# Performance work log

Hardware: AMD Instinct MI355X
Metric: run time of the kernel (lower is better)

The kernel has to match this reference:

```python
import jax, jax.numpy as jnp
import numpy as np

BOX_SIZE = 120
RESOLUTION = 1.0
NUM_NEIGHBOURS = 2
NUM_TYPES = 11
MAX_ATOMS = 512
BATCH = 4


def setup_inputs() -> dict:
    key = jax.random.key(0)
    k1, k2 = jax.random.split(key)
    # coords uniformly inside the box with a margin so Gaussians stay mostly in-grid
    margin = 5.0
    input_coords = jax.random.uniform(
        k1, (BATCH, NUM_TYPES, 3 * MAX_ATOMS), dtype=jnp.float32,
        minval=margin, maxval=BOX_SIZE * RESOLUTION - margin)
    num_atoms = jax.random.randint(k2, (BATCH, NUM_TYPES), 1, MAX_ATOMS + 1).astype(jnp.int64)
    return {"input_coords": input_coords, "num_atoms": num_atoms}


def _coords2volume(input_coords, num_atoms):
    B, T, C = input_coords.shape
    A = C // 3
    pos = input_coords.reshape(B * T, A, 3)  # [BT, A, 3] xyz per atom
    n = NUM_NEIGHBOURS
    res = RESOLUTION
    # (2n+1)^3 neighbour-cell offsets
    r = jnp.arange(-n, n + 1)
    offs = jnp.stack(jnp.meshgrid(r, r, r, indexing="ij"), axis=-1).reshape(-1, 3)  # [K,3]
    # home cell of each atom (spatial hash cell)
    cell = jnp.floor(pos / res).astype(jnp.int32)  # [BT, A, 3]
    nb = cell[:, :, None, :] + offs[None, None, :, :]  # [BT, A, K, 3]
    # truncated Gaussian density at neighbour-cell grid points
    cell_pos = nb.astype(pos.dtype) * res
    r2 = jnp.sum((cell_pos - pos[:, :, None, :]) ** 2, axis=-1)  # [BT, A, K]
    val = jnp.exp(-r2 / (res * res))
    # mask cells outside the grid and padded atoms
    in_box = jnp.all((nb >= 0) & (nb < BOX_SIZE), axis=-1)  # [BT, A, K]
    atom_mask = jnp.arange(A)[None, :] < num_atoms.reshape(-1)[:, None]  # [BT, A]
    val = jnp.where(in_box & atom_mask[:, :, None], val, 0.0)
    # scatter-add into flattened voxel grid
    flat = (nb[..., 0] * BOX_SIZE + nb[..., 1]) * BOX_SIZE + nb[..., 2]
    flat = jnp.clip(flat, 0, BOX_SIZE ** 3 - 1)
    vol = jnp.zeros((B * T, BOX_SIZE ** 3), dtype=pos.dtype)
    bidx = jnp.arange(B * T)[:, None, None]
    vol = vol.at[bidx, flat].add(val)
    return vol.reshape(B, T, BOX_SIZE, BOX_SIZE, BOX_SIZE)


def reference(input_coords, num_atoms):
    return _coords2volume(input_coords, num_atoms)
```

## Files before the change

kernel.cpp:

```cpp
#include <hip/hip_runtime.h>
#include <stdint.h>

#define BOX 120
#define BOX2 (BOX * BOX)
#define BOX3 (BOX * BOX * BOX)
#define NTYPES 11
#define NBATCH 4
#define BT (NBATCH * NTYPES)
#define MAXA 512
#define NNB 2
#define KCELLS 125

#define NBINS (BT * BOX2)
#define BINCAP 8
#define YTILE 8
#define NYT (BOX / YTILE)

#define WS_COUNTS_BYTES ((size_t)NBINS * 4)
#define WS_BINS_BYTES   ((size_t)NBINS * BINCAP * 2)
#define WS_NEEDED       (WS_COUNTS_BYTES + WS_BINS_BYTES)


__global__ __launch_bounds__(256)
void zero_counts_kernel(uint4* __restrict__ counts4, int n4) {
    int i = blockIdx.x * blockDim.x + threadIdx.x;
    if (i < n4) counts4[i] = make_uint4(0u, 0u, 0u, 0u);
}

__global__ __launch_bounds__(256)
void bin_kernel(const float* __restrict__ coords,
                const int* __restrict__ num_atoms,
                uint32_t* __restrict__ counts,
                uint16_t* __restrict__ bins) {
    int tid = blockIdx.x * blockDim.x + threadIdx.x;
    if (tid >= BT * MAXA) return;
    int bt = tid / MAXA;
    int a  = tid % MAXA;
    if (a >= num_atoms[bt]) return;
    const float* p = coords + (size_t)bt * (3 * MAXA) + (size_t)a * 3;
    int cx = (int)floorf(p[0]);
    int cy = (int)floorf(p[1]);
    if ((unsigned)cx >= BOX || (unsigned)cy >= BOX) return;
    int bin = (bt * BOX + cx) * BOX + cy;
    uint32_t idx = atomicAdd(&counts[bin], 1u);
    if (idx < BINCAP) bins[(size_t)bin * BINCAP + idx] = (uint16_t)a;
}

__global__ __launch_bounds__(256)
void gather_kernel(const float* __restrict__ coords,
                   const uint32_t* __restrict__ counts,
                   const uint16_t* __restrict__ bins,
                   float* __restrict__ out) {
    int b  = blockIdx.x;
    int bt = b / (BOX * NYT);
    int r  = b % (BOX * NYT);
    int x  = r / NYT;
    int y0 = (r % NYT) * YTILE;

    const int NB_Y = YTILE + 2 * NNB;
    __shared__ float4 s_at[5 * NB_Y * BINCAP];
    __shared__ float  s_w[5 * NB_Y * BINCAP];
    __shared__ int    s_n;
    if (threadIdx.x == 0) s_n = 0;
    __syncthreads();

    int t = threadIdx.x;
    if (t < 5 * NB_Y) {
        int cxb = x - NNB + t / NB_Y;
        int cyb = y0 - NNB + t % NB_Y;
        if ((unsigned)cxb < BOX && (unsigned)cyb < BOX) {
            int bin = (bt * BOX + cxb) * BOX + cyb;
            int c = (int)counts[bin];
            if (c > BINCAP) c = BINCAP;
            if (c > 0) {
                int base = atomicAdd(&s_n, c);
                for (int k = 0; k < c; ++k) {
                    int a = bins[(size_t)bin * BINCAP + k];
                    const float* p = coords + (size_t)bt * (3 * MAXA) + (size_t)a * 3;
                    float px = p[0], py = p[1], pz = p[2];
                    float fx = (float)x - px;
                    s_at[base + k] = make_float4(py, pz, floorf(py), floorf(pz));
                    s_w[base + k]  = __expf(-fx * fx);
                }
            }
        }
    }
    __syncthreads();
    int n = s_n;

    size_t obase = (size_t)(bt * BOX + x) * BOX2 + (size_t)y0 * BOX;
    for (int it = 0; it < 4; ++it) {
        int v = threadIdx.x + it * 256;
        if (v < YTILE * BOX) {
            float yf = (float)(y0 + v / BOX);
            float zf = (float)(v % BOX);
            float acc = 0.f;
            for (int i = 0; i < n; ++i) {
                float4 at = s_at[i];
                if (fabsf(yf - at.z) <= 2.0f && fabsf(zf - at.w) <= 2.0f) {
                    float dy = yf - at.x;
                    float dz = zf - at.y;
                    acc += s_w[i] * __expf(-(dy * dy + dz * dz));
                }
            }
            __builtin_nontemporal_store(acc, out + obase + v);
        }
    }
}


__global__ __launch_bounds__(256)
void zero_out_kernel(float4* __restrict__ out, int n4) {
    int i = blockIdx.x * blockDim.x + threadIdx.x;
    if (i < n4) out[i] = make_float4(0.f, 0.f, 0.f, 0.f);
}

__global__ __launch_bounds__(256)
void scatter_kernel(const float* __restrict__ coords,
                    const int* __restrict__ num_atoms,
                    float* __restrict__ out) {
    int idx = blockIdx.x * blockDim.x + threadIdx.x;
    const int total = BT * MAXA * KCELLS;
    if (idx >= total) return;
    int k   = idx % KCELLS;
    int tmp = idx / KCELLS;
    int a   = tmp % MAXA;
    int bt  = tmp / MAXA;
    if (a >= num_atoms[bt]) return;
    const float* p = coords + (size_t)bt * (3 * MAXA) + (size_t)a * 3;
    float px = p[0], py = p[1], pz = p[2];
    int dz = k % 5, t2 = k / 5;
    int dy = t2 % 5, dx = t2 / 5;
    int nx = (int)floorf(px) + dx - NNB;
    int ny = (int)floorf(py) + dy - NNB;
    int nz = (int)floorf(pz) + dz - NNB;
    if ((unsigned)nx >= BOX || (unsigned)ny >= BOX || (unsigned)nz >= BOX) return;
    float fx = (float)nx - px, fy = (float)ny - py, fz = (float)nz - pz;
    float val = __expf(-(fx * fx + fy * fy + fz * fz));
    atomicAdd(out + (size_t)bt * BOX3 + (size_t)((nx * BOX + ny) * BOX + nz), val);
}

extern "C" void kernel_launch(void* const* d_in, const int* in_sizes, int n_in,
                              void* d_out, int out_size, void* d_ws, size_t ws_size,
                              hipStream_t stream) {
    const float* coords    = (const float*)d_in[0];
    const int*   num_atoms = (const int*)d_in[1];
    float*       out       = (float*)d_out;

    if (ws_size >= WS_NEEDED) {
        uint32_t* counts = (uint32_t*)d_ws;
        uint16_t* bins   = (uint16_t*)((char*)d_ws + WS_COUNTS_BYTES);

        int n4 = NBINS / 4;
        zero_counts_kernel<<<(n4 + 255) / 256, 256, 0, stream>>>((uint4*)counts, n4);

        bin_kernel<<<(BT * MAXA + 255) / 256, 256, 0, stream>>>(coords, num_atoms, counts, bins);

        int gblocks = BT * BOX * NYT;
        gather_kernel<<<gblocks, 256, 0, stream>>>(coords, counts, bins, out);
    } else {
        int n4 = out_size / 4;
        zero_out_kernel<<<(n4 + 255) / 256, 256, 0, stream>>>((float4*)d_out, n4);
        const int total = BT * MAXA * KCELLS;
        scatter_kernel<<<(total + 255) / 256, 256, 0, stream>>>(coords, num_atoms, out);
    }
}
```

Baseline: 354.6 us.

## Bin atoms by x-slab and gather whole yz planes with threshold culling

Atoms are now binned by x cell only (cap 24 per bin) instead of by (x,y) cell. Each block computes a full 120x120 yz plane for one x slice and writes four voxels per thread as a vector store. Contributions whose separable Gaussian factors fall below a small threshold are skipped, which cuts the per-voxel exp and compare work. The cost is a much larger candidate list per block: with 24 atoms per bin and 5 bins, every voxel scans up to 120 atoms. The threshold also drops tiny values the reference keeps, and bins overflowing 24 atoms silently lose atoms.

```diff
diff --git a/kernel.cpp b/kernel.cpp
--- a/kernel.cpp
+++ b/kernel.cpp
@@ -9,22 +9,22 @@
 #define BT (NBATCH * NTYPES)
 #define MAXA 512
 #define NNB 2
-#define KCELLS 125
 
-#define NBINS (BT * BOX2)
-#define BINCAP 8
-#define YTILE 8
-#define NYT (BOX / YTILE)
+#define DELTA 2e-3f
 
+#define BINCAP 24
+#define NBINS (BT * BOX)
+#define SLOTS (5 * BINCAP)
 #define WS_COUNTS_BYTES ((size_t)NBINS * 4)
 #define WS_BINS_BYTES   ((size_t)NBINS * BINCAP * 2)
 #define WS_NEEDED       (WS_COUNTS_BYTES + WS_BINS_BYTES)
 
+typedef float v4f __attribute__((ext_vector_type(4)));
 
 __global__ __launch_bounds__(256)
-void zero_counts_kernel(uint4* __restrict__ counts4, int n4) {
+void zero_counts_kernel(uint32_t* __restrict__ counts) {
     int i = blockIdx.x * blockDim.x + threadIdx.x;
-    if (i < n4) counts4[i] = make_uint4(0u, 0u, 0u, 0u);
+    if (i < NBINS) counts[i] = 0u;
 }
 
 __global__ __launch_bounds__(256)
@@ -37,50 +37,47 @@
     int bt = tid / MAXA;
     int a  = tid % MAXA;
     if (a >= num_atoms[bt]) return;
-    const float* p = coords + (size_t)bt * (3 * MAXA) + (size_t)a * 3;
-    int cx = (int)floorf(p[0]);
-    int cy = (int)floorf(p[1]);
-    if ((unsigned)cx >= BOX || (unsigned)cy >= BOX) return;
-    int bin = (bt * BOX + cx) * BOX + cy;
-    uint32_t idx = atomicAdd(&counts[bin], 1u);
-    if (idx < BINCAP) bins[(size_t)bin * BINCAP + idx] = (uint16_t)a;
+    float px = coords[(size_t)bt * (3 * MAXA) + 3 * (size_t)a];
+    int cx = (int)floorf(px);
+    if ((unsigned)cx >= BOX) return;
+    int bin = bt * BOX + cx;
+    uint32_t k = atomicAdd(&counts[bin], 1u);
+    if (k < BINCAP) bins[(size_t)bin * BINCAP + k] = (uint16_t)a;
 }
 
 __global__ __launch_bounds__(256)
-void gather_kernel(const float* __restrict__ coords,
-                   const uint32_t* __restrict__ counts,
-                   const uint16_t* __restrict__ bins,
-                   float* __restrict__ out) {
+void gather_slab_kernel(const float* __restrict__ coords,
+                        const uint32_t* __restrict__ counts,
+                        const uint16_t* __restrict__ bins,
+                        v4f* __restrict__ out4) {
     int b  = blockIdx.x;
-    int bt = b / (BOX * NYT);
-    int r  = b % (BOX * NYT);
-    int x  = r / NYT;
-    int y0 = (r % NYT) * YTILE;
+    int bt = b / BOX;
+    int x  = b % BOX;
 
-    const int NB_Y = YTILE + 2 * NNB;
-    __shared__ float4 s_at[5 * NB_Y * BINCAP];
-    __shared__ float  s_w[5 * NB_Y * BINCAP];
+    __shared__ float4 s_at[SLOTS];
+    __shared__ float  s_ex[SLOTS];
     __shared__ int    s_n;
     if (threadIdx.x == 0) s_n = 0;
     __syncthreads();
 
     int t = threadIdx.x;
-    if (t < 5 * NB_Y) {
-        int cxb = x - NNB + t / NB_Y;
-        int cyb = y0 - NNB + t % NB_Y;
-        if ((unsigned)cxb < BOX && (unsigned)cyb < BOX) {
-            int bin = (bt * BOX + cxb) * BOX + cyb;
-            int c = (int)counts[bin];
+    if (t < SLOTS) {
+        int cx = x - NNB + t / BINCAP;
+        int k  = t % BINCAP;
+        if ((unsigned)cx < BOX) {
+            int bin = bt * BOX + cx;
+            uint32_t c = counts[bin];
             if (c > BINCAP) c = BINCAP;
-            if (c > 0) {
-                int base = atomicAdd(&s_n, c);
-                for (int k = 0; k < c; ++k) {
-                    int a = bins[(size_t)bin * BINCAP + k];
-                    const float* p = coords + (size_t)bt * (3 * MAXA) + (size_t)a * 3;
-                    float px = p[0], py = p[1], pz = p[2];
-                    float fx = (float)x - px;
-                    s_at[base + k] = make_float4(py, pz, floorf(py), floorf(pz));
-                    s_w[base + k]  = __expf(-fx * fx);
+            if ((uint32_t)k < c) {
+                int a = bins[(size_t)bin * BINCAP + k];
+                const float* p = coords + (size_t)bt * (3 * MAXA) + 3 * (size_t)a;
+                float px = p[0], py = p[1], pz = p[2];
+                float fx = (float)x - px;
+                float ex = __expf(-fx * fx);
+                if (ex >= DELTA) {
+                    int i = atomicAdd(&s_n, 1);
+                    s_at[i] = make_float4(py, pz, floorf(py), floorf(pz));
+                    s_ex[i] = ex;
                 }
             }
         }
@@ -88,22 +85,33 @@
     __syncthreads();
     int n = s_n;
 
-    size_t obase = (size_t)(bt * BOX + x) * BOX2 + (size_t)y0 * BOX;
-    for (int it = 0; it < 4; ++it) {
-        int v = threadIdx.x + it * 256;
-        if (v < YTILE * BOX) {
-            float yf = (float)(y0 + v / BOX);
-            float zf = (float)(v % BOX);
-            float acc = 0.f;
-            for (int i = 0; i < n; ++i) {
-                float4 at = s_at[i];
-                if (fabsf(yf - at.z) <= 2.0f && fabsf(zf - at.w) <= 2.0f) {
-                    float dy = yf - at.x;
-                    float dz = zf - at.y;
-                    acc += s_w[i] * __expf(-(dy * dy + dz * dz));
+    size_t obase = (size_t)b * (BOX2 / 4);
+    for (int i = 0; i < 15; ++i) {
+        int v4 = threadIdx.x + (i << 8);
+        if (v4 < BOX2 / 4) {
+            int y  = v4 / (BOX / 4);
+            int z0 = (v4 % (BOX / 4)) * 4;
+            float yf = (float)y;
+            float a0 = 0.f, a1 = 0.f, a2 = 0.f, a3 = 0.f;
+            for (int j = 0; j < n; ++j) {
+                float4 at = s_at[j];
+                if (fabsf(yf - at.z) <= 2.0f) {
+                    float dy  = yf - at.x;
+                    float exy = s_ex[j] * __expf(-dy * dy);
+                    if (exy >= DELTA) {
+                        float pz = at.y, fpz = at.w;
+                        float zf = (float)z0;
+                        float dz0 = zf - pz, dz1 = zf + 1.f - pz,
+                              dz2 = zf + 2.f - pz, dz3 = zf + 3.f - pz;
+                        if (fabsf(zf - fpz)        <= 2.0f) a0 += exy * __expf(-dz0 * dz0);
+                        if (fabsf(zf + 1.f - fpz)  <= 2.0f) a1 += exy * __expf(-dz1 * dz1);
+                        if (fabsf(zf + 2.f - fpz)  <= 2.0f) a2 += exy * __expf(-dz2 * dz2);
+                        if (fabsf(zf + 3.f - fpz)  <= 2.0f) a3 += exy * __expf(-dz3 * dz3);
+                    }
                 }
             }
-            __builtin_nontemporal_store(acc, out + obase + v);
+            v4f acc = { a0, a1, a2, a3 };
+            __builtin_nontemporal_store(acc, out4 + obase + v4);
         }
     }
 }
@@ -120,14 +128,14 @@
                     const int* __restrict__ num_atoms,
                     float* __restrict__ out) {
     int idx = blockIdx.x * blockDim.x + threadIdx.x;
-    const int total = BT * MAXA * KCELLS;
+    const int total = BT * MAXA * 125;
     if (idx >= total) return;
-    int k   = idx % KCELLS;
-    int tmp = idx / KCELLS;
+    int k   = idx % 125;
+    int tmp = idx / 125;
     int a   = tmp % MAXA;
     int bt  = tmp / MAXA;
     if (a >= num_atoms[bt]) return;
-    const float* p = coords + (size_t)bt * (3 * MAXA) + (size_t)a * 3;
+    const float* p = coords + (size_t)bt * (3 * MAXA) + 3 * (size_t)a;
     float px = p[0], py = p[1], pz = p[2];
     int dz = k % 5, t2 = k / 5;
     int dy = t2 % 5, dx = t2 / 5;
@@ -145,23 +153,21 @@
                               hipStream_t stream) {
     const float* coords    = (const float*)d_in[0];
     const int*   num_atoms = (const int*)d_in[1];
-    float*       out       = (float*)d_out;
 
     if (ws_size >= WS_NEEDED) {
         uint32_t* counts = (uint32_t*)d_ws;
         uint16_t* bins   = (uint16_t*)((char*)d_ws + WS_COUNTS_BYTES);
 
-        int n4 = NBINS / 4;
-        zero_counts_kernel<<<(n4 + 255) / 256, 256, 0, stream>>>((uint4*)counts, n4);
-
-        bin_kernel<<<(BT * MAXA + 255) / 256, 256, 0, stream>>>(coords, num_atoms, counts, bins);
-
-        int gblocks = BT * BOX * NYT;
-        gather_kernel<<<gblocks, 256, 0, stream>>>(coords, counts, bins, out);
+        zero_counts_kernel<<<(NBINS + 255) / 256, 256, 0, stream>>>(counts);
+        bin_kernel<<<(BT * MAXA + 255) / 256, 256, 0, stream>>>(
+            coords, num_atoms, counts, bins);
+        gather_slab_kernel<<<NBINS, 256, 0, stream>>>(
+            coords, counts, bins, (v4f*)d_out);
     } else {
         int n4 = out_size / 4;
         zero_out_kernel<<<(n4 + 255) / 256, 256, 0, stream>>>((float4*)d_out, n4);
-        const int total = BT * MAXA * KCELLS;
-        scatter_kernel<<<(total + 255) / 256, 256, 0, stream>>>(coords, num_atoms, out);
+        const int total = BT * MAXA * 125;
+        scatter_kernel<<<(total + 255) / 256, 256, 0, stream>>>(
+            coords, num_atoms, (float*)d_out);
     }
 }
```

Result: faster. 330.3 us (-6.8%).
